# Kernel tuning notes

Hardware: AMD Instinct MI355X
Metric: run time of the kernel (lower is better)

## Reference

```python
import jax, jax.numpy as jnp
import numpy as np

H = 100      # STATE_SIZE
ATT = 100    # ATTENTION_SIZE
E = 32       # EMBEDDINGS_SIZE
V = 50257    # char vocab
TV = 60      # tag vocab
N = 2048     # source length (incl EOS padding)
T = 2048     # target length (incl EOS padding)
TT = 64      # number of tags


def lstm_cell(x, h, c, Wih, Whh, b):
    # torch gate order: i, f, g, o
    z = x @ Wih.T + h @ Whh.T + b
    i, f, g, o = jnp.split(z, 4)
    c = jax.nn.sigmoid(f) * c + jax.nn.sigmoid(i) * jnp.tanh(g)
    h = jax.nn.sigmoid(o) * jnp.tanh(c)
    return h, c


def lstm_scan(xs, Wih, Whh, b):
    Hs = Whh.shape[1]
    def step(carry, x):
        h, c = lstm_cell(x, carry[0], carry[1], Wih, Whh, b)
        return (h, c), h
    init = (jnp.zeros(Hs, xs.dtype), jnp.zeros(Hs, xs.dtype))
    _, ys = jax.lax.scan(step, init, xs)
    return ys


def setup_inputs() -> dict:
    key = jax.random.key(0)
    ks = iter(jax.random.split(key, 40))
    def rn(shape, s=0.1):
        return jax.random.normal(next(ks), shape, jnp.float32) * s
    return {
        "src_ids": jax.random.randint(next(ks), (1, N), 0, V),
        "tag_ids": jax.random.randint(next(ks), (1, TT), 0, TV),
        "out_ids": jax.random.randint(next(ks), (1, T), 0, V),
        "weight": jnp.ones((), jnp.float32),
        "emb_char": rn((V, E)),
        "emb_tag": rn((TV, E)),
        "enc_f_Wih": rn((4 * H, E)), "enc_f_Whh": rn((4 * H, H)), "enc_f_b": rn((4 * H,)),
        "enc_b_Wih": rn((4 * H, E)), "enc_b_Whh": rn((4 * H, H)), "enc_b_b": rn((4 * H,)),
        "tag_Wih": rn((4 * H, E)), "tag_Whh": rn((4 * H, H)), "tag_b": rn((4 * H,)),
        "dec_Wih": rn((4 * H, 3 * H + E)), "dec_Whh": rn((4 * H, H)), "dec_b": rn((4 * H,)),
        "attn_w1": rn((ATT, 2 * H)), "attn_w2": rn((ATT, 2 * H)), "attn_w3": rn((ATT, 5)),
        "attn_v": rn((1, ATT)),
        "tag_attn_w1": rn((ATT, H)), "tag_attn_w2": rn((ATT, 2 * H)), "tag_attn_v": rn((1, ATT)),
        "out_W": rn((V, H)), "out_b": rn((V,)),
    }


def reference(src_ids, tag_ids, out_ids, weight, emb_char, emb_tag,
              enc_f_Wih, enc_f_Whh, enc_f_b, enc_b_Wih, enc_b_Whh, enc_b_b,
              tag_Wih, tag_Whh, tag_b, dec_Wih, dec_Whh, dec_b,
              attn_w1, attn_w2, attn_w3, attn_v,
              tag_attn_w1, tag_attn_w2, tag_attn_v, out_W, out_b):
    x = emb_char[src_ids[0]]                       # (N, E)
    tg = emb_tag[tag_ids[0]]                       # (TT, E)
    # bidirectional char encoder
    yf = lstm_scan(x, enc_f_Wih, enc_f_Whh, enc_f_b)
    yb = lstm_scan(x[::-1], enc_b_Wih, enc_b_Whh, enc_b_b)[::-1]
    enc = jnp.concatenate([yf, yb], -1)            # (N, 2H)
    # tag encoder + self-attention residual (matches self_encode_tags)
    tv = lstm_scan(tg, tag_Wih, tag_Whh, tag_b)    # (TT, H)
    sa = jax.nn.softmax(tv @ tv.T, axis=-1)
    tagv = tv + jnp.einsum('sh,st->th', tv, sa)    # (TT, H)
    w1dt = enc @ attn_w1.T                         # (N, ATT)
    tag_w1dt = tagv @ tag_attn_w1.T                # (TT, ATT)
    eos_emb = emb_char[0]
    # initial decoder step on (enc_last, tag_last, eos_emb) with zero state
    x0 = jnp.concatenate([enc[-1], tagv[-1], eos_emb])
    h0, c0 = lstm_cell(x0, jnp.zeros(H, jnp.float32), jnp.zeros(H, jnp.float32),
                       dec_Wih, dec_Whh, dec_b)
    # teacher forcing: previous output embedding (EOS=id 0 at t=0)
    prev_ids = jnp.concatenate([jnp.zeros((1,), out_ids.dtype), out_ids[0, :-1]])
    prev_emb = emb_char[prev_ids]                  # (T, E)

    def step(carry, inp):
        h, c, prev_att = carry
        pe, oid = inp
        state = jnp.concatenate([h, c])            # (2H,)
        # tag attention
        taw = jax.nn.softmax(jnp.tanh(tag_w1dt + state @ tag_attn_w2.T) @ tag_attn_v[0])
        tag_ctx = taw @ tagv                       # (H,)
        new_state = state + jnp.concatenate([tag_ctx, tag_ctx])
        # char attention with 5-wide previous-attention feature
        scores = jnp.tanh(w1dt + new_state @ attn_w2.T + prev_att @ attn_w3.T) @ attn_v[0]
        aw = jax.nn.softmax(scores)                # (N,)
        ctx = aw @ enc                             # (2H,)
        startt = jnp.clip(jnp.argmax(aw) - 1, 0, N - 6)
        new_prev = jax.lax.dynamic_slice(aw, (startt,), (5,))
        hn, cn = lstm_cell(jnp.concatenate([ctx, tag_ctx, pe]), h, c,
                           dec_Wih, dec_Whh, dec_b)
        logits = hn @ out_W.T + out_b              # (V,)
        lt = -jax.nn.log_softmax(logits)[oid]
        return (hn, cn, new_prev), lt

    _, losses = jax.lax.scan(step, (h0, c0, jnp.zeros(5, jnp.float32)),
                             (prev_emb, out_ids[0]))
    return jnp.sum(losses) * weight
```

## Files before the change

### kernel.cpp

```cpp
#include <hip/hip_runtime.h>
#include <math.h>

#define NN   2048
#define TLEN 2048
#define TTAG 64
#define VOC  50257
#define GW   32
#define CHK  64
#define RECU 80
static_assert(GW * CHK == NN, "chunking");

#define OFF_XF    0
#define OFF_XB    (OFF_XF  + NN*400)
#define OFF_TGX   (OFF_XB  + NN*400)
#define OFF_PEW   (OFF_TGX + TTAG*400)
#define OFF_ENC   (OFF_PEW + TLEN*400)
#define OFF_W1DT  (OFF_ENC + NN*200)
#define OFF_TAGV  (OFF_W1DT+ NN*100)
#define OFF_TGW1  (OFF_TAGV+ TTAG*100)
#define OFF_TGW   (OFF_TGW1+ TTAG*100)
#define OFF_HOUT  (OFF_TGW + TTAG*400)
#define OFF_REC   (OFF_HOUT+ TLEN*100)
#define OFF_HC    (OFF_REC + 2*GW*RECU*2)
#define OFF_FLG   (OFF_HC  + 2*128*2)
#define OFF_PB    (OFF_FLG + 4096)


__device__ __forceinline__ float rcpf(float x){ return __builtin_amdgcn_rcpf(x); }
__device__ __forceinline__ float sigf(float x){ return rcpf(1.0f+__expf(-x)); }
__device__ __forceinline__ float tanhfast(float x){
  float e = __expf(2.0f*x);
  return 1.0f - 2.0f*rcpf(e+1.0f);
}
__device__ __forceinline__ unsigned short f2b(float x){
  unsigned b=__float_as_uint(x);
  return (unsigned short)((b + 0x7fffu + ((b>>16)&1u))>>16);
}
__device__ __forceinline__ unsigned pk2(float a,float b){ return (unsigned)f2b(a) | ((unsigned)f2b(b)<<16); }
__device__ __forceinline__ float blo(unsigned u){ return __uint_as_float(u<<16); }
__device__ __forceinline__ float bhi(unsigned u){ return __uint_as_float(u&0xffff0000u); }

__device__ __forceinline__ unsigned long long ald64(const unsigned long long* p){
  return __hip_atomic_load(p,__ATOMIC_RELAXED,__HIP_MEMORY_SCOPE_SYSTEM);
}
__device__ __forceinline__ void ast64(unsigned long long* p, unsigned long long v){
  __hip_atomic_store(p,v,__ATOMIC_RELAXED,__HIP_MEMORY_SCOPE_SYSTEM);
}
__device__ __forceinline__ void vm0(){ asm volatile("s_waitcnt vmcnt(0)" ::: "memory"); }

__global__ void kInit(float* ws){
  unsigned long long* f = (unsigned long long*)(ws + OFF_FLG);
  int i = blockIdx.x*256 + threadIdx.x;
  if (i < 2048) ast64(f+i, 0ull);
}

__global__ __launch_bounds__(512) void kPrep(
    const int* src, const int* tag, const int* oid,
    const float* emb_char, const float* emb_tag,
    const float* fWih, const float* fb,
    const float* bWih, const float* bb,
    const float* tWih, const float* tb,
    const float* dWih, const float* db, float* ws)
{
  int r = blockIdx.x, j = threadIdx.x;
  if (j >= 400) return;
  if (r < NN) {
    const float* e = emb_char + (size_t)src[r]*32;
    const float* Wr = fWih + j*32;
    float a = fb[j];
    #pragma unroll
    for (int q=0;q<32;q++) a += e[q]*Wr[q];
    ws[OFF_XF + r*400 + j] = a;
  } else if (r < 2*NN) {
    int n = r - NN;
    const float* e = emb_char + (size_t)src[n]*32;
    const float* Wr = bWih + j*32;
    float a = bb[j];
    #pragma unroll
    for (int q=0;q<32;q++) a += e[q]*Wr[q];
    ws[OFF_XB + n*400 + j] = a;
  } else if (r < 2*NN + TTAG) {
    int s = r - 2*NN;
    const float* e = emb_tag + (size_t)tag[s]*32;
    const float* Wr = tWih + j*32;
    float a = tb[j];
    #pragma unroll
    for (int q=0;q<32;q++) a += e[q]*Wr[q];
    ws[OFF_TGX + s*400 + j] = a;
  } else {
    int t = r - (2*NN + TTAG);
    int pid = (t==0) ? 0 : oid[t-1];
    const float* e = emb_char + (size_t)pid*32;
    const float* Wr = dWih + (size_t)j*332 + 300;
    float a = db[j];
    #pragma unroll
    for (int q=0;q<32;q++) a += e[q]*Wr[q];
    ws[OFF_PEW + t*400 + j] = a;
  }
}

struct EncShared {
  float tvs[TTAG*100];
  float sa [TTAG*64];
  float hbuf[100];
  float zbuf[400];
};

__device__ void lstm_block(const float* Whh, const float* xbase, float* ws,
                           int reverse, int col, EncShared* sh)
{
  int tid = threadIdx.x;
  float whh[100];
  if (tid < 400){
    #pragma unroll
    for (int k=0;k<100;k++) whh[k] = Whh[tid*100+k];
  }
  float c = 0.f;
  if (tid < 100) sh->hbuf[tid] = 0.f;
  __syncthreads();
  for (int i=0;i<NN;i++){
    int n = reverse ? (NN-1-i) : i;
    if (tid < 400){
      float z = xbase[n*400+tid];
      #pragma unroll
      for (int k=0;k<100;k++) z += whh[k]*sh->hbuf[k];
      sh->zbuf[tid] = z;
    }
    __syncthreads();
    if (tid < 100){
      float zi=sh->zbuf[tid], zf=sh->zbuf[tid+100], zg=sh->zbuf[tid+200], zo=sh->zbuf[tid+300];
      c = sigf(zf)*c + sigf(zi)*tanhfast(zg);
      float h = sigf(zo)*tanhfast(c);
      sh->hbuf[tid] = h;
      ws[OFF_ENC + n*200 + col + tid] = h;
    }
    __syncthreads();
  }
}

__global__ __launch_bounds__(512,1) void kEnc(
    const float* fWhh, const float* bWhh, const float* tWhh,
    const float* taw1, const float* dWih, float* ws)
{
  __shared__ EncShared sh;
  int b = blockIdx.x, tid = threadIdx.x;
  if (b == 0){ lstm_block(fWhh, ws+OFF_XF, ws, 0, 0,   &sh); return; }
  if (b == 1){ lstm_block(bWhh, ws+OFF_XB, ws, 1, 100, &sh); return; }

  {
    float whh[100];
    if (tid<400){
      #pragma unroll
      for (int k=0;k<100;k++) whh[k] = tWhh[tid*100+k];
    }
    float c = 0.f;
    if (tid<100) sh.hbuf[tid] = 0.f;
    __syncthreads();
    for (int s=0;s<TTAG;s++){
      if (tid<400){
        float z = ws[OFF_TGX + s*400 + tid];
        #pragma unroll
        for (int k=0;k<100;k++) z += whh[k]*sh.hbuf[k];
        sh.zbuf[tid] = z;
      }
      __syncthreads();
      if (tid<100){
        float zi=sh.zbuf[tid], zf=sh.zbuf[tid+100], zg=sh.zbuf[tid+200], zo=sh.zbuf[tid+300];
        c = sigf(zf)*c + sigf(zi)*tanhfast(zg);
        float h = sigf(zo)*tanhfast(c);
        sh.hbuf[tid] = h;
        sh.tvs[s*100+tid] = h;
      }
      __syncthreads();
    }
  }
  for (int idx=tid; idx<TTAG*TTAG; idx+=512){
    int s=idx>>6, t2=idx&63;
    float a=0.f;
    #pragma unroll 10
    for (int h=0;h<100;h++) a += sh.tvs[s*100+h]*sh.tvs[t2*100+h];
    sh.sa[idx]=a;
  }
  __syncthreads();
  if (tid<TTAG){
    float m=-1e30f;
    for (int t2=0;t2<64;t2++) m = fmaxf(m, sh.sa[tid*64+t2]);
    float sum=0.f;
    for (int t2=0;t2<64;t2++){ float e=__expf(sh.sa[tid*64+t2]-m); sh.sa[tid*64+t2]=e; sum+=e; }
    float r=1.f/sum;
    for (int t2=0;t2<64;t2++) sh.sa[tid*64+t2]*=r;
  }
  __syncthreads();
  float tvloc[13]; int cnt=0;
  for (int idx=tid; idx<TTAG*100; idx+=512){
    int t2=idx/100, hh=idx%100;
    float a = sh.tvs[t2*100+hh];
    for (int s=0;s<64;s++) a += sh.tvs[s*100+hh]*sh.sa[s*64+t2];
    tvloc[cnt++]=a;
    ws[OFF_TAGV+idx]=a;
  }
  __syncthreads();
  float* tagvs = sh.sa;
  cnt=0;
  for (int idx=tid; idx<TTAG*100; idx+=512) tagvs[idx]=tvloc[cnt++];
  __syncthreads();
  for (int idx=tid; idx<TTAG*100; idx+=512){
    int s=idx/100, k=idx%100;
    float a=0.f;
    #pragma unroll 10
    for (int h=0;h<100;h++) a += tagvs[s*100+h]*taw1[k*100+h];
    ws[OFF_TGW1+idx]=a;
  }
  for (int idx=tid; idx<TTAG*400; idx+=512){
    int s=idx/400, j=idx%400;
    const float* Wr = dWih + (size_t)j*332 + 200;
    float a=0.f;
    #pragma unroll 10
    for (int h=0;h<100;h++) a += tagvs[s*100+h]*Wr[h];
    ws[OFF_TGW+idx]=a;
  }
}

__global__ void kMid(const float* aw1, float* ws){
  __shared__ float er[200];
  int n=blockIdx.x, tid=threadIdx.x;
  for (int i=tid;i<200;i+=128) er[i]=ws[OFF_ENC+n*200+i];
  __syncthreads();
  if (tid<100){
    const float* Wr = aw1 + tid*200;
    float a=0.f;
    #pragma unroll 8
    for (int d=0;d<200;d++) a += er[d]*Wr[d];
    ws[OFF_W1DT + n*100 + tid]=a;
  }
}

__global__ __launch_bounds__(512) void kDec(
    const float* dWhh, const float* dWih,
    const float* aw2, const float* aw3, const float* av,
    const float* taw2, const float* tav, float* ws)
{
  __shared__ unsigned aw2L[100*101];
  __shared__ unsigned tw2L[100*101];
  __shared__ unsigned tw1L[TTAG*51];
  __shared__ unsigned tagvL[TTAG*51];
  __shared__ unsigned w1L[CHK*51];
  __shared__ unsigned encL[CHK*101];
  __shared__ float tavL[100], avL[100], aw3L[500];
  __shared__ float hL[100], cL[100], tcL[100], tsaL[100], nsL[200];
  __shared__ float uL[TTAG], tawL[TTAG];
  __shared__ float ctxL[200], a23L[100], ctxpL[200];
  __shared__ float srowL[CHK], eRL[CHK];
  __shared__ float sclL[GW];
  __shared__ float zOwnL[16];
  __shared__ float hdrL[4];
  __shared__ float prevL[5];
  __shared__ float MS[2];
  __shared__ int   amiL;

  const int tid = threadIdx.x;
  const int w   = blockIdx.x;
  unsigned long long* REC = (unsigned long long*)(ws + OFF_REC);
  unsigned long long* HC  = (unsigned long long*)(ws + OFF_HC);
  unsigned long long* FLG = (unsigned long long*)(ws + OFF_FLG);

  const int nu = (w<4)? 4 : 3;
  const int u0 = (w<4)? w*4 : 16 + (w-4)*3;
  const int nact = nu*4;
  const int jslot = tid>>5, l = tid&31;

  unsigned wca0=0,wca1=0,wca2=0,wca3=0, wha0=0,wha1=0, wta0=0,wta1=0;
  int row=0;
  if (jslot < nact){
    row = (jslot&3)*100 + u0 + (jslot>>2);
    const float* Wr = dWih + (size_t)row*332;
    wca0=pk2(Wr[2*l],Wr[2*l+1]);
    wca1=pk2(Wr[2*(32+l)],Wr[2*(32+l)+1]);
    wca2=pk2(Wr[2*(64+l)],Wr[2*(64+l)+1]);
    if (l<4) wca3=pk2(Wr[2*(96+l)],Wr[2*(96+l)+1]);
    const float* Wh = dWhh + (size_t)row*100;
    wha0=pk2(Wh[2*l],Wh[2*l+1]);
    if (l<18) wha1=pk2(Wh[2*(32+l)],Wh[2*(32+l)+1]);
    const float* Wt = Wr + 200;
    wta0=pk2(Wt[2*l],Wt[2*l+1]);
    if (l<18) wta1=pk2(Wt[2*(32+l)],Wt[2*(32+l)+1]);
  }
  for (int i=tid;i<100*100;i+=512){ int k=i/100,p=i%100; aw2L[k*101+p]=pk2(aw2 [k*200+2*p], aw2 [k*200+2*p+1]); }
  for (int i=tid;i<100*100;i+=512){ int k=i/100,p=i%100; tw2L[k*101+p]=pk2(taw2[k*200+2*p], taw2[k*200+2*p+1]); }
  for (int i=tid;i<TTAG*50;i+=512){ int s=i/50,p=i%50; tw1L[s*51+p]=pk2(ws[OFF_TGW1+s*100+2*p], ws[OFF_TGW1+s*100+2*p+1]); }
  for (int i=tid;i<TTAG*50;i+=512){ int s=i/50,p=i%50; tagvL[s*51+p]=pk2(ws[OFF_TAGV+s*100+2*p], ws[OFF_TAGV+s*100+2*p+1]); }
  for (int i=tid;i<CHK*50;i+=512){ int r=i/50,p=i%50; w1L[r*51+p]=pk2(ws[OFF_W1DT+(w*CHK+r)*100+2*p], ws[OFF_W1DT+(w*CHK+r)*100+2*p+1]); }
  for (int i=tid;i<CHK*100;i+=512){ int r=i/100,p=i%100; encL[r*101+p]=pk2(ws[OFF_ENC+(w*CHK+r)*200+2*p], ws[OFF_ENC+(w*CHK+r)*200+2*p+1]); }
  if (tid<100){ tavL[tid]=tav[tid]; avL[tid]=av[tid]; }
  for (int i=tid;i<500;i+=512) aw3L[i]=aw3[i];
  if (tid<5)   prevL[tid]=0.f;
  if (tid<200) ctxL[tid]=ws[OFF_ENC + 2047*200 + tid];
  __syncthreads();

  if (jslot < nact){
    float acc=0.f;
    { unsigned u=wca0; acc += ctxL[2*l]*blo(u) + ctxL[2*l+1]*bhi(u); }
    { unsigned u=wca1; acc += ctxL[2*(32+l)]*blo(u) + ctxL[2*(32+l)+1]*bhi(u); }
    { unsigned u=wca2; acc += ctxL[2*(64+l)]*blo(u) + ctxL[2*(64+l)+1]*bhi(u); }
    if (l<4){ unsigned u=wca3; acc += ctxL[2*(96+l)]*blo(u) + ctxL[2*(96+l)+1]*bhi(u); }
    acc += __shfl_xor(acc,1,32); acc += __shfl_xor(acc,2,32);
    acc += __shfl_xor(acc,4,32); acc += __shfl_xor(acc,8,32); acc += __shfl_xor(acc,16,32);
    if (l==0) zOwnL[jslot] = acc + ws[OFF_TGW + 63*400 + row] + ws[OFF_PEW + row];
  }
  __syncthreads();
  float cOwn = 0.f;
  if (tid < nu){
    float zi=zOwnL[tid*4+0], zg=zOwnL[tid*4+2], zo=zOwnL[tid*4+3];
    float cc = sigf(zi)*tanhfast(zg);
    float hh = sigf(zo)*tanhfast(cc);
    cOwn = cc;
    ast64(HC + 128 + (u0+tid), (unsigned long long)pk2(hh,cc) | (1ull<<32));
  }

  for (int t=0; t<TLEN; ++t){
    const unsigned sq = (unsigned)(t+1);
    unsigned long long* slot = REC + (size_t)(t&1)*GW*RECU;
    unsigned long long* hcg  = HC + (size_t)((t+1)&1)*128;
    unsigned long long* hcp  = HC + (size_t)(t&1)*128;
    unsigned long long* fr   = FLG + (size_t)(t&1)*GW*16;
    unsigned long long* fh   = FLG + (size_t)(64 + (t&1)*GW)*16;

    if (tid < 100){
      const unsigned long long* p0 = hcg + tid;
      unsigned long long v;
      for(;;){ v=ald64(p0); if((unsigned)(v>>32)==sq) break; __builtin_amdgcn_s_sleep(1); }
      unsigned lo=(unsigned)v;
      hL[tid]=blo(lo); cL[tid]=bhi(lo);
    }
    __syncthreads();
    if (tid<400){
      int k=tid>>2, q=tid&3, off=q*50;
      const float* sb = (off<100)? (hL+off) : (cL+(off-100));
      float acc=0.f;
      #pragma unroll
      for (int i=0;i<25;i++){ unsigned u=tw2L[k*101+q*25+i]; acc += sb[2*i]*blo(u) + sb[2*i+1]*bhi(u); }
      acc += __shfl_xor(acc,1,4); acc += __shfl_xor(acc,2,4);
      if (q==0) tsaL[k]=acc;
    }
    __syncthreads();
    {
      int sp=tid>>3, l8=tid&7;
      float acc=0.f;
      for (int k=l8;k<100;k+=8){
        unsigned u=tw1L[sp*51+(k>>1)];
        float w1v=(k&1)? bhi(u) : blo(u);
        acc += tanhfast(w1v + tsaL[k]) * tavL[k];
      }
      acc += __shfl_xor(acc,1,8); acc += __shfl_xor(acc,2,8); acc += __shfl_xor(acc,4,8);
      if (l8==0) uL[sp]=acc;
    }
    __syncthreads();
    if (tid<64){
      float v=uL[tid], m=v;
      for (int d=1;d<64;d<<=1) m=fmaxf(m,__shfl_xor(m,d,64));
      float e=__expf(v-m), ssum=e;
      for (int d=1;d<64;d<<=1) ssum+=__shfl_xor(ssum,d,64);
      tawL[tid]=e*rcpf(ssum);
    }
    __syncthreads();
    if (tid<400){
      int hh=tid>>2, q=tid&3;
      float acc=0.f;
      #pragma unroll
      for (int i=0;i<16;i++){
        int s=q*16+i;
        unsigned u=tagvL[s*51+(hh>>1)];
        acc += tawL[s]*((hh&1)? bhi(u):blo(u));
      }
      acc += __shfl_xor(acc,1,4); acc += __shfl_xor(acc,2,4);
      if (q==0){ tcL[hh]=acc; nsL[hh]=hL[hh]+acc; nsL[100+hh]=cL[hh]+acc; }
    }
    __syncthreads();
    if (tid<400){
      int k=tid>>2, q=tid&3, off=q*50;
      float acc=0.f;
      #pragma unroll
      for (int i=0;i<25;i++){ unsigned u=aw2L[k*101+q*25+i]; acc += nsL[off+2*i]*blo(u) + nsL[off+2*i+1]*bhi(u); }
      acc += __shfl_xor(acc,1,4); acc += __shfl_xor(acc,2,4);
      if (q==0){
        float a3=0.f;
        #pragma unroll
        for (int i=0;i<5;i++) a3 += prevL[i]*aw3L[k*5+i];
        a23L[k]=acc+a3;
      }
    }
    __syncthreads();
    {
      int r=tid>>3, l8=tid&7;
      float acc=0.f;
      for (int k=l8;k<100;k+=8){
        unsigned u=w1L[r*51+(k>>1)];
        float w1v=(k&1)? bhi(u) : blo(u);
        acc += tanhfast(w1v + a23L[k]) * avL[k];
      }
      acc += __shfl_xor(acc,1,8); acc += __shfl_xor(acc,2,8); acc += __shfl_xor(acc,4,8);
      if (l8==0) srowL[r]=acc;
    }
    __syncthreads();
    if (tid<64){
      float v=srowL[tid], m=v;
      for (int d=1;d<64;d<<=1) m=fmaxf(m,__shfl_xor(m,d,64));
      float e=__expf(v-m); eRL[tid]=e;
      float Ss=e;
      for (int d=1;d<64;d<<=1) Ss+=__shfl_xor(Ss,d,64);
      float bv=v; int bi=w*CHK+tid;
      for (int d=1;d<64;d<<=1){
        float ov=__shfl_xor(bv,d,64); int oi=__shfl_xor(bi,d,64);
        if (ov>bv || (ov==bv && oi<bi)){ bv=ov; bi=oi; }
      }
      if (tid==0){ hdrL[0]=m; hdrL[1]=Ss; hdrL[2]=bv; ((int*)hdrL)[3]=bi; }
    }
    __syncthreads();
    if (tid<400){
      int d=tid>>1, hf=tid&1;
      float acc=0.f;
      #pragma unroll 8
      for (int i=0;i<32;i++){
        int rr=hf*32+i;
        unsigned u=encL[rr*101+(d>>1)];
        acc += eRL[rr]*((d&1)? bhi(u):blo(u));
      }
      acc += __shfl_xor(acc,1,2);
      if (hf==0) ctxpL[d]=acc;
    } else if (tid>=448){
      int lane = tid-448;
      unsigned long long* rp = slot + (size_t)w*RECU;
      if (lane < 16){ int j=lane;
        ast64(rp+50+j, (unsigned long long)pk2(srowL[4*j],srowL[4*j+1])
                     | ((unsigned long long)pk2(srowL[4*j+2],srowL[4*j+3])<<32));
      } else if (lane==16)
        ast64(rp+66, (unsigned long long)__float_as_uint(hdrL[0])
                   | ((unsigned long long)__float_as_uint(hdrL[1])<<32));
      else if (lane==17)
        ast64(rp+67, (unsigned long long)__float_as_uint(hdrL[2])
                   | ((unsigned long long)(unsigned)((int*)hdrL)[3]<<32));
      vm0();
      if (lane==0) ast64(fh + (size_t)w*16, (unsigned long long)sq);
    }
    __syncthreads();

    #define ZPRE_ROW() do{ \
      if (jslot < nact){ \
        float acc=0.f; \
        { unsigned u=wha0; acc += hL[2*l]*blo(u) + hL[2*l+1]*bhi(u); } \
        if (l<18){ unsigned u=wha1; acc += hL[2*(32+l)]*blo(u) + hL[2*(32+l)+1]*bhi(u); } \
        { unsigned u=wta0; acc += tcL[2*l]*blo(u) + tcL[2*l+1]*bhi(u); } \
        if (l<18){ unsigned u=wta1; acc += tcL[2*(32+l)]*blo(u) + tcL[2*(32+l)+1]*bhi(u); } \
        acc += __shfl_xor(acc,1,32); acc += __shfl_xor(acc,2,32); \
        acc += __shfl_xor(acc,4,32); acc += __shfl_xor(acc,8,32); acc += __shfl_xor(acc,16,32); \
        if (l==0) zOwnL[jslot] = acc + ws[OFF_PEW + t*400 + row]; \
      } \
    }while(0)

    if (tid < 448){
      ZPRE_ROW();
    } else {
      int lane = tid-448;
      unsigned long long* rp = slot + (size_t)w*RECU;
      if (lane < 50)
        ast64(rp+lane, (unsigned long long)pk2(ctxpL[4*lane],ctxpL[4*lane+1])
                     | ((unsigned long long)pk2(ctxpL[4*lane+2],ctxpL[4*lane+3])<<32));
      vm0();
      if (lane==0) ast64(fr + (size_t)w*16, (unsigned long long)sq);
      ZPRE_ROW();
    }

    if (tid < 64){
      int ok = (tid >= GW) ? 1 : 0;
      for(;;){
        if (!ok) ok = ((unsigned)ald64(fh + (size_t)tid*16) == sq);
        if (__all(ok)) break;
      }
    }
    __syncthreads();
    if (tid < 64){
      int ok = (tid >= GW) ? 1 : 0;
      for(;;){
        if (!ok) ok = ((unsigned)ald64(fr + (size_t)tid*16) == sq);
        if (__all(ok)) break;
      }
    } else if (tid>=448){
      int lane=tid-448, r=lane&31, up=lane>>5;
      unsigned long long v = ald64(slot + (size_t)r*RECU + 66 + up);
      float x0 = __uint_as_float((unsigned)v);
      float x1 = __uint_as_float((unsigned)(v>>32));
      int   xi = (int)(unsigned)(v>>32);
      float pv = x0; int pi = xi;
      #pragma unroll
      for (int d=1;d<32;d<<=1){
        float ov=__shfl_xor(pv,d,32); int oi=__shfl_xor(pi,d,32);
        if (up){ if (ov>pv || (ov==pv && oi<pi)){ pv=ov; pi=oi; } }
        else   { pv = fmaxf(pv,ov); }
      }
      if (!up){
        float sc = __expf(x0 - pv);
        sclL[r] = sc;
        float ss = sc * x1;
        #pragma unroll
        for (int d=1;d<32;d<<=1) ss += __shfl_xor(ss,d,32);
        if (r==0){ MS[0]=pv; MS[1]=ss; }
      } else {
        if (r==0) amiL = pi;
      }
    }
    __syncthreads();
    if (tid<400){
      float rS = rcpf(MS[1]);
      int dw=tid>>3, s8=tid&7;
      float c0=0.f,c1=0.f,c2=0.f,c3=0.f;
      #pragma unroll
      for (int i=0;i<4;i++){
        unsigned long long p = ald64(slot + (size_t)(s8*4+i)*RECU + dw);
        float sc = sclL[s8*4+i];
        unsigned lo=(unsigned)p, hi=(unsigned)(p>>32);
        c0 += blo(lo)*sc; c1 += bhi(lo)*sc;
        c2 += blo(hi)*sc; c3 += bhi(hi)*sc;
      }
      #pragma unroll
      for (int d=1;d<8;d<<=1){
        c0 += __shfl_xor(c0,d,8); c1 += __shfl_xor(c1,d,8);
        c2 += __shfl_xor(c2,d,8); c3 += __shfl_xor(c3,d,8);
      }
      if (s8==0){
        ctxL[4*dw+0]=c0*rS; ctxL[4*dw+1]=c1*rS;
        ctxL[4*dw+2]=c2*rS; ctxL[4*dw+3]=c3*rS;
      }
    }
    __syncthreads();
    if (jslot < nact){
      float acc=0.f;
      { unsigned u=wca0; acc += ctxL[2*l]*blo(u) + ctxL[2*l+1]*bhi(u); }
      { unsigned u=wca1; acc += ctxL[2*(32+l)]*blo(u) + ctxL[2*(32+l)+1]*bhi(u); }
      { unsigned u=wca2; acc += ctxL[2*(64+l)]*blo(u) + ctxL[2*(64+l)+1]*bhi(u); }
      if (l<4){ unsigned u=wca3; acc += ctxL[2*(96+l)]*blo(u) + ctxL[2*(96+l)+1]*bhi(u); }
      acc += __shfl_xor(acc,1,32); acc += __shfl_xor(acc,2,32);
      acc += __shfl_xor(acc,4,32); acc += __shfl_xor(acc,8,32); acc += __shfl_xor(acc,16,32);
      if (l==0) zOwnL[jslot] += acc;
    }
    __syncthreads();
    if (tid>=440 && tid<445){
      int i=tid-440;
      int st = amiL-1; st = st<0?0:st; st = st>NN-6?NN-6:st;
      int g = st+i, r=g>>6, lr=g&63;
      unsigned long long v = ald64(slot + (size_t)r*RECU + 50 + (lr>>2));
      unsigned half = (lr&2)? (unsigned)(v>>32) : (unsigned)v;
      float sc = (lr&1)? bhi(half) : blo(half);
      prevL[i] = __expf(sc - MS[0]) * rcpf(MS[1]);
    }
    if (tid < nu){
      float zi=zOwnL[tid*4+0], zf=zOwnL[tid*4+1], zg=zOwnL[tid*4+2], zo=zOwnL[tid*4+3];
      float cc = sigf(zf)*cOwn + sigf(zi)*tanhfast(zg);
      float hh = sigf(zo)*tanhfast(cc);
      cOwn = cc;
      ast64(hcp + (u0+tid), (unsigned long long)pk2(hh,cc)
                          | ((unsigned long long)(sq+1)<<32));
      ws[OFF_HOUT + t*100 + (u0+tid)] = hh;
    }
  }
}

__global__ __launch_bounds__(256) void kLoss(const float* outW, const float* outb,
                                             const int* oid, float* ws)
{
  const int b=blockIdx.x, tid=threadIdx.x;
  const int tile=b>>1, hf=b&1, t0=tile*16;
  __shared__ float s_hn[16*100];
  __shared__ int   s_oid[16];
  __shared__ float red[4][16][3];
  for (int i=tid;i<1600;i+=256) s_hn[i]=ws[OFF_HOUT + t0*100 + i];
  if (tid<16) s_oid[tid]=oid[t0+tid];
  __syncthreads();
  const int VSPLIT = 25129;
  int vbeg = hf? VSPLIT : 0;
  int vend = hf? VOC : VSPLIT;
  float rm[16], rs[16], ol[16];
  #pragma unroll
  for (int tt=0;tt<16;tt++){ rm[tt]=-1e30f; rs[tt]=0.f; ol[tt]=-1e30f; }
  for (int v=vbeg+tid; v<vend; v+=256){
    const float4* wr = (const float4*)(outW + (size_t)v*100);
    float acc[16];
    #pragma unroll
    for (int tt=0;tt<16;tt++) acc[tt]=0.f;
    #pragma unroll 5
    for (int q=0;q<25;q++){
      float4 wv = wr[q];
      #pragma unroll
      for (int tt=0;tt<16;tt++){
        float4 hv = *(const float4*)(s_hn + tt*100 + q*4);
        acc[tt] += wv.x*hv.x + wv.y*hv.y + wv.z*hv.z + wv.w*hv.w;
      }
    }
    float bb = outb[v];
    #pragma unroll
    for (int tt=0;tt<16;tt++){
      float lg = acc[tt] + bb;
      if (v == s_oid[tt]) ol[tt] = fmaxf(ol[tt], lg);
      if (lg <= rm[tt]) rs[tt] += __expf(lg - rm[tt]);
      else { rs[tt] = rs[tt]*__expf(rm[tt]-lg) + 1.0f; rm[tt]=lg; }
    }
  }
  int wv2=tid>>6, ln=tid&63;
  #pragma unroll
  for (int tt=0;tt<16;tt++){
    float m=rm[tt], sv=rs[tt], o=ol[tt];
    for (int d=1;d<64;d<<=1){
      float om=__shfl_xor(m,d,64), os=__shfl_xor(sv,d,64), oo=__shfl_xor(o,d,64);
      float M2=fmaxf(m,om);
      sv = sv*__expf(m-M2) + os*__expf(om-M2);
      m=M2; o=fmaxf(o,oo);
    }
    if (ln==0){ red[wv2][tt][0]=m; red[wv2][tt][1]=sv; red[wv2][tt][2]=o; }
  }
  __syncthreads();
  if (tid<16){
    float M=-1e30f;
    for (int q=0;q<4;q++) M=fmaxf(M,red[q][tid][0]);
    float S=0.f, O=-1e30f;
    for (int q=0;q<4;q++){ S += red[q][tid][1]*__expf(red[q][tid][0]-M); O=fmaxf(O,red[q][tid][2]); }
    float* pb = ws + OFF_PB + (((tile*2)+hf)*16 + tid)*4;
    pb[0]=M; pb[1]=S; pb[2]=O;
  }
}

__global__ void kFinal(const float* weight, float* ws, float* out){
  __shared__ float red[256];
  int tid=threadIdx.x;
  float acc=0.f;
  for (int t=tid;t<TLEN;t+=256){
    int tile=t>>4, tt=t&15;
    const float* p0 = ws + OFF_PB + ((tile*2+0)*16+tt)*4;
    const float* p1 = ws + OFF_PB + ((tile*2+1)*16+tt)*4;
    float M=fmaxf(p0[0],p1[0]);
    float S=p0[1]*__expf(p0[0]-M) + p1[1]*__expf(p1[0]-M);
    float O=fmaxf(p0[2],p1[2]);
    acc += (M + logf(S)) - O;
  }
  red[tid]=acc; __syncthreads();
  for (int d=128; d>0; d>>=1){
    if (tid<d) red[tid]+=red[tid+d];
    __syncthreads();
  }
  if (tid==0) out[0]=red[0]*weight[0];
}

extern "C" void kernel_launch(void* const* d_in, const int* in_sizes, int n_in,
                              void* d_out, int out_size, void* d_ws, size_t ws_size,
                              hipStream_t stream) {
  const int*   src      = (const int*)  d_in[0];
  const int*   tag      = (const int*)  d_in[1];
  const int*   oid      = (const int*)  d_in[2];
  const float* weight   = (const float*)d_in[3];
  const float* emb_char = (const float*)d_in[4];
  const float* emb_tag  = (const float*)d_in[5];
  const float* fWih=(const float*)d_in[6],  *fWhh=(const float*)d_in[7],  *fb=(const float*)d_in[8];
  const float* bWih=(const float*)d_in[9],  *bWhh=(const float*)d_in[10], *bb=(const float*)d_in[11];
  const float* tWih=(const float*)d_in[12], *tWhh=(const float*)d_in[13], *tb=(const float*)d_in[14];
  const float* dWih=(const float*)d_in[15], *dWhh=(const float*)d_in[16], *db=(const float*)d_in[17];
  const float* aw1 =(const float*)d_in[18], *aw2=(const float*)d_in[19];
  const float* aw3 =(const float*)d_in[20], *av =(const float*)d_in[21];
  const float* taw1=(const float*)d_in[22], *taw2=(const float*)d_in[23], *tavv=(const float*)d_in[24];
  const float* outW=(const float*)d_in[25], *outb=(const float*)d_in[26];
  float* ws  = (float*)d_ws;
  float* out = (float*)d_out;

  kInit<<<8, 256, 0, stream>>>(ws);
  kPrep<<<2*NN+TTAG+TLEN, 512, 0, stream>>>(src,tag,oid,emb_char,emb_tag,
                                            fWih,fb,bWih,bb,tWih,tb,dWih,db,ws);
  kEnc<<<3,512,0,stream>>>(fWhh,bWhh,tWhh,taw1,dWih,ws);
  kMid<<<NN,128,0,stream>>>(aw1,ws);
  kDec<<<GW,512,0,stream>>>(dWhh,dWih,aw2,aw3,av,taw2,tavv,ws);
  kLoss<<<256,256,0,stream>>>(outW,outb,oid,ws);
  kFinal<<<1,256,0,stream>>>(weight,ws,out);
}
```

Before: 25.91 ms.

## Drop max-subtraction in attention softmax and merge cross-block flag waits

The decoder attention softmax no longer subtracts the per-chunk and global max. Each block writes unnormalized exp(score) and its sum, and context partials are summed directly without rescaling, which removes one __syncthreads phase and the per-chunk rescale factors. The two flag waits are restructured so the header-flag wait runs on the tail warp with s_sleep, overlapping the partial-context flag wait. This risks overflow or loss of precision if scores grow large, since exp is taken without max stabilization. Scores are bounded by the tanh sum times v, so in practice it may be safe.

After: 24.94 ms (median of 2 runs). 1.04x faster.

```diff
diff --git a/kernel.cpp b/kernel.cpp
--- a/kernel.cpp
+++ b/kernel.cpp
@@ -251,11 +251,9 @@
   __shared__ float uL[TTAG], tawL[TTAG];
   __shared__ float ctxL[200], a23L[100], ctxpL[200];
   __shared__ float srowL[CHK], eRL[CHK];
-  __shared__ float sclL[GW];
   __shared__ float zOwnL[16];
-  __shared__ float hdrL[4];
   __shared__ float prevL[5];
-  __shared__ float MS[2];
+  __shared__ float Sg;
   __shared__ int   amiL;
 
   const int tid = threadIdx.x;
@@ -399,21 +397,7 @@
         acc += tanhfast(w1v + a23L[k]) * avL[k];
       }
       acc += __shfl_xor(acc,1,8); acc += __shfl_xor(acc,2,8); acc += __shfl_xor(acc,4,8);
-      if (l8==0) srowL[r]=acc;
-    }
-    __syncthreads();
-    if (tid<64){
-      float v=srowL[tid], m=v;
-      for (int d=1;d<64;d<<=1) m=fmaxf(m,__shfl_xor(m,d,64));
-      float e=__expf(v-m); eRL[tid]=e;
-      float Ss=e;
-      for (int d=1;d<64;d<<=1) Ss+=__shfl_xor(Ss,d,64);
-      float bv=v; int bi=w*CHK+tid;
-      for (int d=1;d<64;d<<=1){
-        float ov=__shfl_xor(bv,d,64); int oi=__shfl_xor(bi,d,64);
-        if (ov>bv || (ov==bv && oi<bi)){ bv=ov; bi=oi; }
-      }
-      if (tid==0){ hdrL[0]=m; hdrL[1]=Ss; hdrL[2]=bv; ((int*)hdrL)[3]=bi; }
+      if (l8==0){ srowL[r]=acc; eRL[r]=__expf(acc); }
     }
     __syncthreads();
     if (tid<400){
@@ -429,16 +413,24 @@
       if (hf==0) ctxpL[d]=acc;
     } else if (tid>=448){
       int lane = tid-448;
+      float eS = eRL[lane];
+      float sv = srowL[lane]; int si = w*CHK+lane;
+      #pragma unroll
+      for (int d=1;d<64;d<<=1){
+        eS += __shfl_xor(eS,d,64);
+        float ov=__shfl_xor(sv,d,64); int oi=__shfl_xor(si,d,64);
+        if (ov>sv || (ov==sv && oi<si)){ sv=ov; si=oi; }
+      }
       unsigned long long* rp = slot + (size_t)w*RECU;
       if (lane < 16){ int j=lane;
         ast64(rp+50+j, (unsigned long long)pk2(srowL[4*j],srowL[4*j+1])
                      | ((unsigned long long)pk2(srowL[4*j+2],srowL[4*j+3])<<32));
       } else if (lane==16)
-        ast64(rp+66, (unsigned long long)__float_as_uint(hdrL[0])
-                   | ((unsigned long long)__float_as_uint(hdrL[1])<<32));
+        ast64(rp+66, (unsigned long long)__float_as_uint(eS)
+                   | ((unsigned long long)__float_as_uint(sv)<<32));
       else if (lane==17)
-        ast64(rp+67, (unsigned long long)__float_as_uint(hdrL[2])
-                   | ((unsigned long long)(unsigned)((int*)hdrL)[3]<<32));
+        ast64(rp+67, (unsigned long long)__float_as_uint(sv)
+                   | ((unsigned long long)(unsigned)si<<32));
       vm0();
       if (lane==0) ast64(fh + (size_t)w*16, (unsigned long long)sq);
     }
@@ -459,6 +451,13 @@
 
     if (tid < 448){
       ZPRE_ROW();
+      if (tid < 64){
+        int ok = (tid >= GW) ? 1 : 0;
+        for(;;){
+          if (!ok) ok = ((unsigned)ald64(fr + (size_t)tid*16) == sq);
+          if (__all(ok)) break;
+        }
+      }
     } else {
       int lane = tid-448;
       unsigned long long* rp = slot + (size_t)w*RECU;
@@ -468,58 +467,39 @@
       vm0();
       if (lane==0) ast64(fr + (size_t)w*16, (unsigned long long)sq);
       ZPRE_ROW();
-    }
-
-    if (tid < 64){
-      int ok = (tid >= GW) ? 1 : 0;
-      for(;;){
-        if (!ok) ok = ((unsigned)ald64(fh + (size_t)tid*16) == sq);
-        if (__all(ok)) break;
-      }
-    }
-    __syncthreads();
-    if (tid < 64){
-      int ok = (tid >= GW) ? 1 : 0;
-      for(;;){
-        if (!ok) ok = ((unsigned)ald64(fr + (size_t)tid*16) == sq);
-        if (__all(ok)) break;
-      }
-    } else if (tid>=448){
-      int lane=tid-448, r=lane&31, up=lane>>5;
-      unsigned long long v = ald64(slot + (size_t)r*RECU + 66 + up);
-      float x0 = __uint_as_float((unsigned)v);
-      float x1 = __uint_as_float((unsigned)(v>>32));
-      int   xi = (int)(unsigned)(v>>32);
-      float pv = x0; int pi = xi;
-      #pragma unroll
-      for (int d=1;d<32;d<<=1){
-        float ov=__shfl_xor(pv,d,32); int oi=__shfl_xor(pi,d,32);
-        if (up){ if (ov>pv || (ov==pv && oi<pi)){ pv=ov; pi=oi; } }
-        else   { pv = fmaxf(pv,ov); }
-      }
-      if (!up){
-        float sc = __expf(x0 - pv);
-        sclL[r] = sc;
-        float ss = sc * x1;
-        #pragma unroll
-        for (int d=1;d<32;d<<=1) ss += __shfl_xor(ss,d,32);
-        if (r==0){ MS[0]=pv; MS[1]=ss; }
-      } else {
-        if (r==0) amiL = pi;
+      {
+        int r = lane&31, up = lane>>5;
+        const unsigned long long* fp = fh + (size_t)r*16;
+        for(;;){ if ((unsigned)ald64(fp)==sq) break; __builtin_amdgcn_s_sleep(1); }
+        unsigned long long v = ald64(slot + (size_t)r*RECU + 66 + up);
+        if (!up){
+          float ss = __uint_as_float((unsigned)v);
+          #pragma unroll
+          for (int d=1;d<32;d<<=1) ss += __shfl_xor(ss,d,32);
+          if (r==0) Sg = ss;
+        } else {
+          float pv = __uint_as_float((unsigned)v);
+          int   pi = (int)(unsigned)(v>>32);
+          #pragma unroll
+          for (int d=1;d<32;d<<=1){
+            float ov=__shfl_xor(pv,d,32); int oi=__shfl_xor(pi,d,32);
+            if (ov>pv || (ov==pv && oi<pi)){ pv=ov; pi=oi; }
+          }
+          if (r==0) amiL = pi;
+        }
       }
     }
     __syncthreads();
     if (tid<400){
-      float rS = rcpf(MS[1]);
+      float rS = rcpf(Sg);
       int dw=tid>>3, s8=tid&7;
       float c0=0.f,c1=0.f,c2=0.f,c3=0.f;
       #pragma unroll
       for (int i=0;i<4;i++){
         unsigned long long p = ald64(slot + (size_t)(s8*4+i)*RECU + dw);
-        float sc = sclL[s8*4+i];
         unsigned lo=(unsigned)p, hi=(unsigned)(p>>32);
-        c0 += blo(lo)*sc; c1 += bhi(lo)*sc;
-        c2 += blo(hi)*sc; c3 += bhi(hi)*sc;
+        c0 += blo(lo); c1 += bhi(lo);
+        c2 += blo(hi); c3 += bhi(hi);
       }
       #pragma unroll
       for (int d=1;d<8;d<<=1){
@@ -550,7 +530,7 @@
       unsigned long long v = ald64(slot + (size_t)r*RECU + 50 + (lr>>2));
       unsigned half = (lr&2)? (unsigned)(v>>32) : (unsigned)v;
       float sc = (lr&1)? bhi(half) : blo(half);
-      prevL[i] = __expf(sc - MS[0]) * rcpf(MS[1]);
+      prevL[i] = __expf(sc) * rcpf(Sg);
     }
     if (tid < nu){
       float zi=zOwnL[tid*4+0], zf=zOwnL[tid*4+1], zg=zOwnL[tid*4+2], zo=zOwnL[tid*4+3];
```
